# Performance work log

Measured on AMD Instinct MI355X. Metric: run time of the kernel, lower is better.

Reference implementation:

```python
import jax, jax.numpy as jnp
import numpy as np

B, S = 1, 4096
H, KV, D, HID = 8, 4, 256, 2304   # heads, kv heads, head_dim, hidden_size
G = H // KV                        # GQA group size
WINDOW = 1024                      # sliding window
THETA = 10000.0                    # rope_local_base_freq (sliding attention)
EPS = 1e-6
SCALE = 256.0 ** -0.5              # query_pre_attn_scalar ** -0.5


def rms_norm(x, w, eps=EPS):
    # Gemma3RMSNorm: fp32 rms over last dim, scale by (1 + weight)
    v = jnp.mean(jnp.square(x), axis=-1, keepdims=True)
    return x * jax.lax.rsqrt(v + eps) * (1.0 + w)


def rope(x, position_ids):
    # x: [B, S, N, D]; split-half rotation as in Gemma3RotaryEmbedding
    d = x.shape[-1]
    inv_freq = 1.0 / (THETA ** (jnp.arange(0, d, 2, dtype=jnp.float32) / d))  # [D/2]
    freqs = position_ids.astype(jnp.float32)[:, :, None] * inv_freq  # [B, S, D/2]
    cos = jnp.cos(freqs)[:, :, None, :]  # [B, S, 1, D/2]
    sin = jnp.sin(freqs)[:, :, None, :]
    x1, x2 = jnp.split(x, 2, axis=-1)
    return jnp.concatenate([x1 * cos - x2 * sin, x1 * sin + x2 * cos], axis=-1)


def setup_inputs() -> dict:
    key = jax.random.key(0)
    ks = jax.random.split(key, 6)
    n = lambda k, shp, sc: jax.random.normal(k, shp, dtype=jnp.float32) * sc
    return {
        "x": n(ks[0], (B, S, HID), 1.0),
        "position_ids": jnp.broadcast_to(jnp.arange(S, dtype=jnp.int32)[None, :], (B, S)),
        "wq": n(ks[1], (HID, H * D), 0.02),
        "wk": n(ks[2], (HID, KV * D), 0.02),
        "wv": n(ks[3], (HID, KV * D), 0.02),
        "wo": n(ks[4], (H * D, HID), 0.02),
        "q_norm_w": jnp.zeros((D,), dtype=jnp.float32),
        "k_norm_w": jnp.zeros((D,), dtype=jnp.float32),
    }


def reference(x, position_ids, wq, wk, wv, wo, q_norm_w, k_norm_w):
    b, s, _ = x.shape
    q = (x @ wq).reshape(b, s, H, D)
    k = (x @ wk).reshape(b, s, KV, D)
    v = (x @ wv).reshape(b, s, KV, D)

    # QK-RMSNorm over head_dim, then RoPE, then query scaling
    q = rms_norm(q, q_norm_w)
    k = rms_norm(k, k_norm_w)
    q = rope(q, position_ids)
    k = rope(k, position_ids)
    q = q * SCALE

    # GQA: group queries over shared KV heads. qg: [B, S, KV, G, D]
    qg = q.reshape(b, s, KV, G, D)
    scores = jnp.einsum('bqcgd,btcd->bcgqt', qg, k)  # [B, KV, G, S, S]

    # causal + sliding-window mask: t <= q and q - t < WINDOW
    pi = position_ids[:, :, None]  # query positions [B, S, 1]
    pj = position_ids[:, None, :]  # key positions   [B, 1, S]
    mask = (pj <= pi) & (pi - pj < WINDOW)  # [B, S, S]
    neg = jnp.finfo(scores.dtype).min
    scores = jnp.where(mask[:, None, None, :, :], scores, neg)

    probs = jax.nn.softmax(scores, axis=-1)
    out = jnp.einsum('bcgqt,btcd->bqcgd', probs, v).reshape(b, s, H * D)
    return out @ wo
```

## Files before the change

kernel.cpp:

```cpp
#include <hip/hip_runtime.h>
#include <stdint.h>

typedef unsigned short u16;
typedef __attribute__((ext_vector_type(8))) short bf16x8;
typedef __attribute__((ext_vector_type(4))) float f32x4;

#define S_LEN 4096
#define HID_DIM 2304
#define QKV_N 4096
#define AO_N 2048
#define HD 256
#define WIN 1024
#define QSCALE 0.0625f

static __device__ __forceinline__ u16 f2bf(float f) {
  union { float f; uint32_t u; } v; v.f = f;
  return (u16)((v.u + 0x7FFFu + ((v.u >> 16) & 1u)) >> 16);
}
static __device__ __forceinline__ float bf2f(u16 h) {
  union { uint32_t u; float f; } v; v.u = ((uint32_t)h) << 16;
  return v.f;
}

static __device__ __forceinline__ void gld16(const void* src, void* dst) {
  __builtin_amdgcn_global_load_lds((const __attribute__((address_space(1))) void*)src,
                                   (__attribute__((address_space(3))) void*)dst, 16, 0, 0);
}

#define BAR() __builtin_amdgcn_s_barrier()
#define LG0() asm volatile("s_waitcnt lgkmcnt(0)" ::: "memory")
#define VM4() asm volatile("s_waitcnt vmcnt(4)" ::: "memory")
#define VM2() asm volatile("s_waitcnt vmcnt(2)" ::: "memory")
#define VM0() asm volatile("s_waitcnt vmcnt(0)" ::: "memory")
#define PRIO1() __builtin_amdgcn_s_setprio(1)
#define PRIO0() __builtin_amdgcn_s_setprio(0)

__global__ __launch_bounds__(256) void k_cvt_bf16(const float* __restrict__ in,
                                                  u16* __restrict__ out, int n) {
  int i = (blockIdx.x * 256 + threadIdx.x) * 4;
  if (i >= n) return;
  float4 v = *(const float4*)(in + i);
  uint64_t p = (uint64_t)f2bf(v.x) | ((uint64_t)f2bf(v.y) << 16)
             | ((uint64_t)f2bf(v.z) << 32) | ((uint64_t)f2bf(v.w) << 48);
  *(uint64_t*)(out + i) = p;
}

__global__ __launch_bounds__(256) void k_transpose_cvt(const float* __restrict__ in, int C,
                                                       u16* __restrict__ out, int out_stride,
                                                       int row_off) {
  __shared__ float tile[32][33];
  int c0 = blockIdx.x * 32, r0 = blockIdx.y * 32;
  int tx = threadIdx.x & 31, ty = threadIdx.x >> 5;
#pragma unroll
  for (int i = 0; i < 4; i++)
    tile[ty + i * 8][tx] = in[(size_t)(r0 + ty + i * 8) * C + c0 + tx];
  __syncthreads();
#pragma unroll
  for (int i = 0; i < 4; i++)
    out[(size_t)(row_off + c0 + ty + i * 8) * out_stride + r0 + tx] = f2bf(tile[tx][ty + i * 8]);
}

__global__ __launch_bounds__(256) void k_vtrans(const u16* __restrict__ qkv,
                                                u16* __restrict__ vtout) {
  __shared__ u16 tile[32][33];
  int c0 = blockIdx.x * 32, s0 = blockIdx.y * 32;
  int tx = threadIdx.x & 31, ty = threadIdx.x >> 5;
#pragma unroll
  for (int i = 0; i < 4; i++)
    tile[ty + i * 8][tx] = qkv[(size_t)(s0 + ty + i * 8) * QKV_N + 3072 + c0 + tx];
  __syncthreads();
#pragma unroll
  for (int i = 0; i < 4; i++)
    vtout[(size_t)(c0 + ty + i * 8) * S_LEN + s0 + tx] = tile[tx][ty + i * 8];
}

template <int OUT_BF16>
__global__ __launch_bounds__(512, 2) void k_gemm8p(const u16* __restrict__ A,
                                                   const u16* __restrict__ Bt,
                                                   void* __restrict__ Cout,
                                                   int M, int N, int K) {
  __shared__ u16 sA[2][256 * 64];
  __shared__ u16 sB[2][256 * 64];
  const int t = threadIdx.x, lane = t & 63, wave = t >> 6;
  const int wr = wave >> 2, wc = wave & 3;
  const int l15 = lane & 15, l4 = lane >> 4;
  const int nbn = N >> 8;
  const int cpx = gridDim.x >> 3;
  const int wg = ((int)blockIdx.x & 7) * cpx + ((int)blockIdx.x >> 3);
  const int bm = wg / nbn, bn = wg % nbn;
  const int NT = K >> 6;
  const int srow = lane >> 3;
  const int sslot = ((lane & 7) ^ srow) * 8;
  const u16* Abase = A + (size_t)(bm * 256) * K;
  const u16* Bbase = Bt + (size_t)(bn * 256) * K;
  f32x4 acc[8][4] = {};
  bf16x8 aF[4][2], b01[2][2], b23[2][2];

#define STG_A(BUF, HALF, KT) do {                                                 \
    _Pragma("unroll")                                                             \
    for (int c_ = 0; c_ < 2; c_++) {                                              \
      int rb_ = (HALF) * 128 + (wave * 2 + c_) * 8;                               \
      gld16(Abase + (size_t)(rb_ + srow) * K + ((KT) << 6) + sslot,               \
            &sA[BUF][rb_ * 64]);                                                  \
    }                                                                             \
  } while (0)
#define STG_B(BUF, HALF, KT) do {                                                 \
    _Pragma("unroll")                                                             \
    for (int c_ = 0; c_ < 2; c_++) {                                              \
      int rb_ = (HALF) * 128 + (wave * 2 + c_) * 8;                               \
      gld16(Bbase + (size_t)(rb_ + srow) * K + ((KT) << 6) + sslot,               \
            &sB[BUF][rb_ * 64]);                                                  \
    }                                                                             \
  } while (0)
#define LDA(BUF, M_, KK)                                                          \
  (*(const bf16x8*)&sA[BUF][((M_) * 32 + wr * 16 + l15) * 64 +                    \
                            ((((KK) << 2) + l4) ^ (l15 & 7)) * 8])
#define LDB(BUF, N_, KK)                                                          \
  (*(const bf16x8*)&sB[BUF][((N_) * 64 + wc * 16 + l15) * 64 +                    \
                            ((((KK) << 2) + l4) ^ (l15 & 7)) * 8])

#define P1_LOADS(b_) do {                                                         \
    _Pragma("unroll") for (int m_ = 0; m_ < 4; m_++)                              \
      _Pragma("unroll") for (int k_ = 0; k_ < 2; k_++)                            \
        aF[m_][k_] = LDA(b_, m_, k_);                                             \
    _Pragma("unroll") for (int n_ = 0; n_ < 2; n_++)                              \
      _Pragma("unroll") for (int k_ = 0; k_ < 2; k_++)                            \
        b01[n_][k_] = LDB(b_, n_, k_);                                            \
  } while (0)
#define P2_LOADS(b_) do {                                                         \
    _Pragma("unroll") for (int n_ = 0; n_ < 2; n_++)                              \
      _Pragma("unroll") for (int k_ = 0; k_ < 2; k_++)                            \
        b23[n_][k_] = LDB(b_, n_ + 2, k_);                                        \
  } while (0)
#define P3_LOADS(b_) do {                                                         \
    _Pragma("unroll") for (int m_ = 0; m_ < 4; m_++)                              \
      _Pragma("unroll") for (int k_ = 0; k_ < 2; k_++)                            \
        aF[m_][k_] = LDA(b_, m_ + 4, k_);                                         \
  } while (0)
#define MFMA16(MOFF, NOFF, BREG) do {                                             \
    _Pragma("unroll") for (int m_ = 0; m_ < 4; m_++)                              \
      _Pragma("unroll") for (int n_ = 0; n_ < 2; n_++)                            \
        _Pragma("unroll") for (int k_ = 0; k_ < 2; k_++)                          \
          acc[m_ + MOFF][n_ + NOFF] = __builtin_amdgcn_mfma_f32_16x16x32_bf16(    \
              aF[m_][k_], BREG[n_][k_], acc[m_ + MOFF][n_ + NOFF], 0, 0, 0);      \
  } while (0)

  STG_A(0, 0, 0);
  STG_B(0, 0, 0);
  STG_B(0, 1, 0);
  STG_A(0, 1, 0);
  VM4();
  BAR();

  for (int tt = 0; tt < NT - 1; ++tt) {
    const int b = tt & 1, nb = b ^ 1;
    P1_LOADS(b);
    STG_A(nb, 0, tt + 1);
    BAR(); LG0(); PRIO1(); MFMA16(0, 0, b01); PRIO0();
    VM4();
    BAR();
    P2_LOADS(b);
    STG_B(nb, 0, tt + 1);
    BAR(); LG0(); PRIO1(); MFMA16(0, 2, b23); PRIO0();
    VM4();
    BAR();
    P3_LOADS(b);
    STG_B(nb, 1, tt + 1);
    BAR(); LG0(); PRIO1(); MFMA16(4, 0, b01); PRIO0();
    BAR();
    STG_A(nb, 1, tt + 1);
    BAR(); PRIO1(); MFMA16(4, 2, b23); PRIO0();
    VM4();
    BAR();
  }
  {
    const int b = (NT - 1) & 1;
    P1_LOADS(b);
    BAR(); LG0(); PRIO1(); MFMA16(0, 0, b01); PRIO0();
    VM2();
    BAR();
    P2_LOADS(b);
    BAR(); LG0(); PRIO1(); MFMA16(0, 2, b23); PRIO0();
    VM0();
    BAR();
    P3_LOADS(b);
    BAR(); LG0(); PRIO1(); MFMA16(4, 0, b01); PRIO0();
    BAR();
    PRIO1(); MFMA16(4, 2, b23); PRIO0();
  }

#pragma unroll
  for (int m = 0; m < 8; m++)
#pragma unroll
    for (int n = 0; n < 4; n++)
#pragma unroll
      for (int r = 0; r < 4; r++) {
        size_t row = bm * 256 + m * 32 + wr * 16 + l4 * 4 + r;
        size_t col = bn * 256 + n * 64 + wc * 16 + l15;
        if (OUT_BF16)
          ((u16*)Cout)[row * N + col] = f2bf(acc[m][n][r]);
        else
          ((float*)Cout)[row * N + col] = acc[m][n][r];
      }
#undef STG_A
#undef STG_B
#undef LDA
#undef LDB
#undef P1_LOADS
#undef P2_LOADS
#undef P3_LOADS
#undef MFMA16
}

__global__ __launch_bounds__(128) void k_normrope(u16* __restrict__ qkv,
                                                  const int* __restrict__ pos_ids,
                                                  const float* __restrict__ qw,
                                                  const float* __restrict__ kw) {
  __shared__ float cross[2];
  int idx = blockIdx.x;
  int s = idx / 12, r = idx % 12;
  bool is_q = (r < 8);
  u16* p = qkv + (size_t)s * QKV_N + (is_q ? r * HD : 2048 + (r - 8) * HD);
  const float* w = is_q ? qw : kw;
  int j = threadIdx.x;
  float x1 = bf2f(p[j]), x2 = bf2f(p[j + 128]);
  float ss = x1 * x1 + x2 * x2;
#pragma unroll
  for (int off = 1; off < 64; off <<= 1) ss += __shfl_xor(ss, off);
  if ((threadIdx.x & 63) == 0) cross[threadIdx.x >> 6] = ss;
  __syncthreads();
  float rms = rsqrtf((cross[0] + cross[1]) * (1.0f / 256.0f) + 1e-6f);
  float y1 = x1 * rms * (1.0f + w[j]);
  float y2 = x2 * rms * (1.0f + w[j + 128]);
  float ang = (float)pos_ids[s] * exp2f((float)j * (-13.287712379549449f / 128.0f));
  float sn, c;
  sincosf(ang, &sn, &c);
  float sc = is_q ? QSCALE : 1.0f;
  p[j] = f2bf((y1 * c - y2 * sn) * sc);
  p[j + 128] = f2bf((y1 * sn + y2 * c) * sc);
}

__global__ __launch_bounds__(256, 2) void k_attn(const u16* __restrict__ qkv,
                                                 const u16* __restrict__ vt,
                                                 const int* __restrict__ pos_ids,
                                                 u16* __restrict__ aout) {
  __shared__ u16 lK[64 * 256];
  __shared__ u16 lV[256 * 64];
  __shared__ u16 lP[4][16 * 64];
  const int bid = blockIdx.x;
  const int wg = (bid & 7) * 64 + (bid >> 3);
  const int kvh = wg >> 7;
  const int q0 = (wg & 127) * 32;
  const int t = threadIdx.x, lane = t & 63, wave = t >> 6;
  const int l15 = lane & 15, l4 = lane >> 4;
  const int head = kvh * 2 + (wave >> 1);
  const int qw = q0 + (wave & 1) * 16;

  bf16x8 qfr[8];
  {
    const u16* qptr = qkv + (size_t)(qw + l15) * QKV_N + head * HD + l4 * 8;
#pragma unroll
    for (int kc = 0; kc < 8; kc++) qfr[kc] = *(const bf16x8*)(qptr + kc * 32);
  }
  f32x4 acc[16] = {};
  float mrow[4], lrow[4];
#pragma unroll
  for (int r = 0; r < 4; r++) { mrow[r] = -1e30f; lrow[r] = 0.0f; }
  int qi[4];
#pragma unroll
  for (int r = 0; r < 4; r++) qi[r] = pos_ids[qw + l4 * 4 + r];

  const int krw = lane >> 5, kcl = lane & 31;
  const int vrw = lane >> 3, vcl = lane & 7;
  const u16* kgb = qkv + 2048 + kvh * HD;
  const u16* vgb = vt + (size_t)kvh * HD * S_LEN;

  int start = q0 - (WIN - 1);
  if (start < 0) start = 0;
  start &= ~63;

#define STAGE_KV(T0) do {                                                             \
    _Pragma("unroll")                                                                 \
    for (int i_ = 0; i_ < 8; i_++) {                                                  \
      int ch_ = wave * 8 + i_;                                                        \
      int kr_ = ch_ * 2 + krw;                                                        \
      gld16(kgb + (size_t)((T0) + kr_) * QKV_N + ((kcl ^ (kr_ & 7)) * 8),             \
            &lK[ch_ * 512]);                                                          \
      int vr_ = ch_ * 8 + vrw;                                                        \
      gld16(vgb + (size_t)vr_ * S_LEN + (T0) + ((vcl ^ (vr_ & 7)) * 8),               \
            &lV[ch_ * 512]);                                                          \
    }                                                                                 \
  } while (0)

  for (int t0 = start; t0 <= q0 + 31; t0 += 64) {
    STAGE_KV(t0);
    int kp[4];
#pragma unroll
    for (int kb = 0; kb < 4; kb++) kp[kb] = pos_ids[t0 + kb * 16 + l15];
    __syncthreads();
    f32x4 sv[4] = {};
    PRIO1();
#pragma unroll
    for (int kb = 0; kb < 4; kb++) {
      const char* krow = (const char*)&lK[(kb * 16 + l15) * 256];
      const int sw = ((kb * 16 + l15) & 7) << 4;
#pragma unroll
      for (int kc = 0; kc < 8; kc++) {
        bf16x8 kf = *(const bf16x8*)(krow + ((kc * 64 + l4 * 16) ^ sw));
        sv[kb] = __builtin_amdgcn_mfma_f32_16x16x32_bf16(qfr[kc], kf, sv[kb], 0, 0, 0);
      }
    }
    PRIO0();
    float sloc[4][4], mx[4];
    float need = 0.0f;
#pragma unroll
    for (int r = 0; r < 4; r++) {
      int pi = qi[r];
#pragma unroll
      for (int kb = 0; kb < 4; kb++)
        sloc[r][kb] = ((kp[kb] <= pi) && (pi - kp[kb] < WIN)) ? sv[kb][r] : -__builtin_inff();
      float m_ = fmaxf(fmaxf(sloc[r][0], sloc[r][1]), fmaxf(sloc[r][2], sloc[r][3]));
#pragma unroll
      for (int off = 1; off < 16; off <<= 1) m_ = fmaxf(m_, __shfl_xor(m_, off));
      mx[r] = m_;
      need = fmaxf(need, m_ - mrow[r]);
    }
    bool resc = __any(need > 8.0f);
    if (resc) {
#pragma unroll
      for (int r = 0; r < 4; r++) {
        float nm = fmaxf(mrow[r], mx[r]);
        float al = __expf(mrow[r] - nm);
        mrow[r] = nm;
        lrow[r] *= al;
#pragma unroll
        for (int nd = 0; nd < 16; nd++) acc[nd][r] *= al;
      }
    }
#pragma unroll
    for (int r = 0; r < 4; r++) {
      float nm = mrow[r];
      float e0 = __expf(sloc[r][0] - nm), e1 = __expf(sloc[r][1] - nm);
      float e2 = __expf(sloc[r][2] - nm), e3 = __expf(sloc[r][3] - nm);
      float sum = (e0 + e1) + (e2 + e3);
#pragma unroll
      for (int off = 1; off < 16; off <<= 1) sum += __shfl_xor(sum, off);
      lrow[r] += sum;
      int q = l4 * 4 + r;
      char* lpw = (char*)&lP[wave][0] + q * 128;
      int swp = (q & 7) << 4;
      *(u16*)(lpw + ((l15 * 2) ^ swp)) = f2bf(e0);
      *(u16*)(lpw + ((32 + l15 * 2) ^ swp)) = f2bf(e1);
      *(u16*)(lpw + ((64 + l15 * 2) ^ swp)) = f2bf(e2);
      *(u16*)(lpw + ((96 + l15 * 2) ^ swp)) = f2bf(e3);
    }
#pragma unroll
    for (int kc2 = 0; kc2 < 2; kc2++) {
      int q = l15;
      bf16x8 pa = *(const bf16x8*)((const char*)&lP[wave][0] + q * 128 +
                                   ((kc2 * 64 + l4 * 16) ^ ((q & 7) << 4)));
      PRIO1();
#pragma unroll
      for (int nd = 0; nd < 16; nd++) {
        int d = nd * 16 + l15;
        bf16x8 vf = *(const bf16x8*)((const char*)&lV[d * 64] +
                                     ((kc2 * 64 + l4 * 16) ^ ((d & 7) << 4)));
        acc[nd] = __builtin_amdgcn_mfma_f32_16x16x32_bf16(pa, vf, acc[nd], 0, 0, 0);
      }
      PRIO0();
    }
    __syncthreads();
  }
  float rinv[4];
#pragma unroll
  for (int r = 0; r < 4; r++) rinv[r] = 1.0f / lrow[r];
#pragma unroll
  for (int nd = 0; nd < 16; nd++)
#pragma unroll
    for (int r = 0; r < 4; r++) {
      size_t row = qw + l4 * 4 + r;
      aout[row * AO_N + head * HD + nd * 16 + l15] = f2bf(acc[nd][r] * rinv[r]);
    }
#undef STAGE_KV
}

extern "C" void kernel_launch(void* const* d_in, const int* in_sizes, int n_in,
                              void* d_out, int out_size, void* d_ws, size_t ws_size,
                              hipStream_t stream) {
  const float* x = (const float*)d_in[0];
  const int* pos = (const int*)d_in[1];
  const float* wq = (const float*)d_in[2];
  const float* wk = (const float*)d_in[3];
  const float* wv = (const float*)d_in[4];
  const float* wo = (const float*)d_in[5];
  const float* qnw = (const float*)d_in[6];
  const float* knw = (const float*)d_in[7];

  u16* qkv = (u16*)d_out;
  u16* xbf = (u16*)d_ws;
  u16* wT = (u16*)((char*)d_ws + 18874368);
  u16* vtb = (u16*)((char*)d_ws + 28311552);
  u16* aout = xbf;

  k_cvt_bf16<<<9216, 256, 0, stream>>>(x, xbf, S_LEN * HID_DIM);
  k_transpose_cvt<<<dim3(64, 72), 256, 0, stream>>>(wq, 2048, wT, HID_DIM, 0);
  k_transpose_cvt<<<dim3(32, 72), 256, 0, stream>>>(wk, 1024, wT, HID_DIM, 2048);
  k_transpose_cvt<<<dim3(32, 72), 256, 0, stream>>>(wv, 1024, wT, HID_DIM, 3072);
  k_gemm8p<1><<<dim3(256), 512, 0, stream>>>(xbf, wT, qkv, S_LEN, QKV_N, HID_DIM);
  k_vtrans<<<dim3(32, 128), 256, 0, stream>>>(qkv, vtb);
  k_normrope<<<S_LEN * 12, 128, 0, stream>>>(qkv, pos, qnw, knw);
  k_attn<<<dim3(512), 256, 0, stream>>>(qkv, vtb, pos, aout);
  k_transpose_cvt<<<dim3(72, 64), 256, 0, stream>>>(wo, HID_DIM, wT, 2048, 0);
  k_gemm8p<0><<<dim3(144), 512, 0, stream>>>(aout, wT, d_out, S_LEN, HID_DIM, 2048);
}
```

Baseline: 266.6 us.

## Fuse QK RMSNorm and RoPE into QKV GEMM epilogue, merge weight transposes

The QKV projection GEMM now applies per-head RMSNorm, RoPE and the query scale directly in its epilogue for the Q and K column blocks. It stages accumulator rows through shared memory and writes packed bf16. This removes the separate normrope kernel and its extra read-modify-write pass over Q and K. The three wq/wk/wv transposes are merged into a single launch, and the wo transpose moves ahead of attention. The cost is a heavier, more synchronised GEMM epilogue with sincos evaluated per element.

```diff
diff --git a/kernel.cpp b/kernel.cpp
--- a/kernel.cpp
+++ b/kernel.cpp
@@ -60,6 +60,32 @@
     out[(size_t)(row_off + c0 + ty + i * 8) * out_stride + r0 + tx] = f2bf(tile[tx][ty + i * 8]);
 }
 
+__global__ __launch_bounds__(256) void k_transpose_w(const float* __restrict__ wq,
+                                                     const float* __restrict__ wk,
+                                                     const float* __restrict__ wv,
+                                                     u16* __restrict__ out) {
+  int ct = blockIdx.x;
+  int r0 = blockIdx.y * 32;
+  const float* src;
+  int C, c0;
+  if (ct < 64) {
+    src = wq; C = 2048; c0 = ct * 32;
+  } else if (ct < 96) {
+    src = wk; C = 1024; c0 = (ct - 64) * 32;
+  } else {
+    src = wv; C = 1024; c0 = (ct - 96) * 32;
+  }
+  __shared__ float tile[32][33];
+  int tx = threadIdx.x & 31, ty = threadIdx.x >> 5;
+#pragma unroll
+  for (int i = 0; i < 4; i++)
+    tile[ty + i * 8][tx] = src[(size_t)(r0 + ty + i * 8) * C + c0 + tx];
+  __syncthreads();
+#pragma unroll
+  for (int i = 0; i < 4; i++)
+    out[(size_t)(ct * 32 + ty + i * 8) * HID_DIM + r0 + tx] = f2bf(tile[tx][ty + i * 8]);
+}
+
 __global__ __launch_bounds__(256) void k_vtrans(const u16* __restrict__ qkv,
                                                 u16* __restrict__ vtout) {
   __shared__ u16 tile[32][33];
@@ -74,11 +100,14 @@
     vtout[(size_t)(c0 + ty + i * 8) * S_LEN + s0 + tx] = tile[tx][ty + i * 8];
 }
 
-template <int OUT_BF16>
+template <int MODE>
 __global__ __launch_bounds__(512, 2) void k_gemm8p(const u16* __restrict__ A,
                                                    const u16* __restrict__ Bt,
                                                    void* __restrict__ Cout,
-                                                   int M, int N, int K) {
+                                                   int M, int N, int K,
+                                                   const int* __restrict__ pos_ids,
+                                                   const float* __restrict__ qnw,
+                                                   const float* __restrict__ knw) {
   __shared__ u16 sA[2][256 * 64];
   __shared__ u16 sB[2][256 * 64];
   const int t = threadIdx.x, lane = t & 63, wave = t >> 6;
@@ -189,19 +218,64 @@
     PRIO1(); MFMA16(4, 2, b23); PRIO0();
   }
 
-#pragma unroll
-  for (int m = 0; m < 8; m++)
-#pragma unroll
-    for (int n = 0; n < 4; n++)
-#pragma unroll
-      for (int r = 0; r < 4; r++) {
-        size_t row = bm * 256 + m * 32 + wr * 16 + l4 * 4 + r;
-        size_t col = bn * 256 + n * 64 + wc * 16 + l15;
-        if (OUT_BF16)
-          ((u16*)Cout)[row * N + col] = f2bf(acc[m][n][r]);
-        else
-          ((float*)Cout)[row * N + col] = acc[m][n][r];
+  if (MODE == 1 && bn < 12) {
+    const float* wvec = (bn < 8) ? qnw : knw;
+    const float scl = (bn < 8) ? QSCALE : 1.0f;
+    float* slab = (float*)&sA[0][0];
+    __syncthreads();
+#pragma unroll
+    for (int m = 0; m < 8; m++) {
+#pragma unroll
+      for (int n = 0; n < 4; n++)
+#pragma unroll
+        for (int r = 0; r < 4; r++)
+          slab[(wr * 16 + l4 * 4 + r) * 264 + n * 64 + wc * 16 + l15] = acc[m][n][r];
+      __syncthreads();
+#pragma unroll
+      for (int rr = 0; rr < 4; rr++) {
+        int lrow = wave * 4 + rr;
+        int grow = bm * 256 + m * 32 + lrow;
+        f32x4 v = *(const f32x4*)&slab[lrow * 264 + lane * 4];
+        float ss = v[0] * v[0] + v[1] * v[1] + v[2] * v[2] + v[3] * v[3];
+#pragma unroll
+        for (int off = 1; off < 64; off <<= 1) ss += __shfl_xor(ss, off);
+        float rms = rsqrtf(ss * (1.0f / 256.0f) + 1e-6f);
+        f32x4 wv4 = *(const f32x4*)&wvec[lane * 4];
+        float y[4], yo[4];
+#pragma unroll
+        for (int j = 0; j < 4; j++) y[j] = v[j] * rms * (1.0f + wv4[j]);
+#pragma unroll
+        for (int j = 0; j < 4; j++) yo[j] = __shfl_xor(y[j], 32);
+        int pos = pos_ids[grow];
+        uint64_t pk = 0;
+#pragma unroll
+        for (int j = 0; j < 4; j++) {
+          int jj = (lane & 31) * 4 + j;
+          float ang = (float)pos * exp2f((float)jj * (-13.287712379549449f / 128.0f));
+          float sn, cs;
+          sincosf(ang, &sn, &cs);
+          float o = (lane < 32) ? (y[j] * cs - yo[j] * sn) : (yo[j] * sn + y[j] * cs);
+          pk |= (uint64_t)f2bf(o * scl) << (16 * j);
+        }
+        *(uint64_t*)&((u16*)Cout)[(size_t)grow * N + bn * 256 + lane * 4] = pk;
       }
+      __syncthreads();
+    }
+  } else {
+#pragma unroll
+    for (int m = 0; m < 8; m++)
+#pragma unroll
+      for (int n = 0; n < 4; n++)
+#pragma unroll
+        for (int r = 0; r < 4; r++) {
+          size_t row = bm * 256 + m * 32 + wr * 16 + l4 * 4 + r;
+          size_t col = bn * 256 + n * 64 + wc * 16 + l15;
+          if (MODE == 1)
+            ((u16*)Cout)[row * N + col] = f2bf(acc[m][n][r]);
+          else
+            ((float*)Cout)[row * N + col] = acc[m][n][r];
+        }
+  }
 #undef STG_A
 #undef STG_B
 #undef LDA
@@ -210,34 +284,6 @@
 #undef P2_LOADS
 #undef P3_LOADS
 #undef MFMA16
-}
-
-__global__ __launch_bounds__(128) void k_normrope(u16* __restrict__ qkv,
-                                                  const int* __restrict__ pos_ids,
-                                                  const float* __restrict__ qw,
-                                                  const float* __restrict__ kw) {
-  __shared__ float cross[2];
-  int idx = blockIdx.x;
-  int s = idx / 12, r = idx % 12;
-  bool is_q = (r < 8);
-  u16* p = qkv + (size_t)s * QKV_N + (is_q ? r * HD : 2048 + (r - 8) * HD);
-  const float* w = is_q ? qw : kw;
-  int j = threadIdx.x;
-  float x1 = bf2f(p[j]), x2 = bf2f(p[j + 128]);
-  float ss = x1 * x1 + x2 * x2;
-#pragma unroll
-  for (int off = 1; off < 64; off <<= 1) ss += __shfl_xor(ss, off);
-  if ((threadIdx.x & 63) == 0) cross[threadIdx.x >> 6] = ss;
-  __syncthreads();
-  float rms = rsqrtf((cross[0] + cross[1]) * (1.0f / 256.0f) + 1e-6f);
-  float y1 = x1 * rms * (1.0f + w[j]);
-  float y2 = x2 * rms * (1.0f + w[j + 128]);
-  float ang = (float)pos_ids[s] * exp2f((float)j * (-13.287712379549449f / 128.0f));
-  float sn, c;
-  sincosf(ang, &sn, &c);
-  float sc = is_q ? QSCALE : 1.0f;
-  p[j] = f2bf((y1 * c - y2 * sn) * sc);
-  p[j + 128] = f2bf((y1 * sn + y2 * c) * sc);
 }
 
 __global__ __launch_bounds__(256, 2) void k_attn(const u16* __restrict__ qkv,
@@ -403,13 +449,12 @@
   u16* aout = xbf;
 
   k_cvt_bf16<<<9216, 256, 0, stream>>>(x, xbf, S_LEN * HID_DIM);
-  k_transpose_cvt<<<dim3(64, 72), 256, 0, stream>>>(wq, 2048, wT, HID_DIM, 0);
-  k_transpose_cvt<<<dim3(32, 72), 256, 0, stream>>>(wk, 1024, wT, HID_DIM, 2048);
-  k_transpose_cvt<<<dim3(32, 72), 256, 0, stream>>>(wv, 1024, wT, HID_DIM, 3072);
-  k_gemm8p<1><<<dim3(256), 512, 0, stream>>>(xbf, wT, qkv, S_LEN, QKV_N, HID_DIM);
+  k_transpose_w<<<dim3(128, 72), 256, 0, stream>>>(wq, wk, wv, wT);
+  k_gemm8p<1><<<dim3(256), 512, 0, stream>>>(xbf, wT, qkv, S_LEN, QKV_N, HID_DIM,
+                                             pos, qnw, knw);
   k_vtrans<<<dim3(32, 128), 256, 0, stream>>>(qkv, vtb);
-  k_normrope<<<S_LEN * 12, 128, 0, stream>>>(qkv, pos, qnw, knw);
+  k_transpose_cvt<<<dim3(72, 64), 256, 0, stream>>>(wo, HID_DIM, wT, 2048, 0);
   k_attn<<<dim3(512), 256, 0, stream>>>(qkv, vtb, pos, aout);
-  k_transpose_cvt<<<dim3(72, 64), 256, 0, stream>>>(wo, HID_DIM, wT, 2048, 0);
-  k_gemm8p<0><<<dim3(144), 512, 0, stream>>>(aout, wT, d_out, S_LEN, HID_DIM, 2048);
-}
+  k_gemm8p<0><<<dim3(144), 512, 0, stream>>>(aout, wT, d_out, S_LEN, HID_DIM, 2048,
+                                             nullptr, nullptr, nullptr);
+}
```

New measurement: 305.7 us. 1.15x slower.
